# Optimization experiments

Hardware: AMD Instinct MI355X
Metric: run time of the kernel (lower is better)

## Reference

```python
import jax, jax.numpy as jnp
import numpy as np

DIM = 2048
NUM_HEADS = 16
HEAD_DIM = DIM // NUM_HEADS
FF_MULT = 2
ROPE_BASE = 10000.0
EPS = 1e-6


def _rmsnorm(x, g):
    return x * jax.lax.rsqrt(jnp.mean(x * x, axis=-1, keepdims=True) + EPS) * g


def _rope_tables(seq_len):
    half = HEAD_DIM // 2
    inv_freq = 1.0 / (ROPE_BASE ** (2.0 * jnp.arange(half, dtype=jnp.float32) / HEAD_DIM))
    angles = jnp.arange(seq_len, dtype=jnp.float32)[:, None] * inv_freq[None, :]  # (S, half)
    return jnp.cos(angles), jnp.sin(angles)


def _apply_rope(x, cos, sin):
    # x: (B, H, S, D); cos/sin: (S, D/2). Interleaved pairs (RoFormer form).
    x_even = x[..., 0::2]
    x_odd = x[..., 1::2]
    c = cos[None, None].astype(x.dtype)
    s = sin[None, None].astype(x.dtype)
    rot_even = x_even * c - x_odd * s
    rot_odd = x_odd * c + x_even * s
    return jnp.stack([rot_even, rot_odd], axis=-1).reshape(x.shape)


def setup_inputs() -> dict:
    key = jax.random.key(0)
    ks = jax.random.split(key, 7)
    B, S = 2, 2048
    scale = 1.0 / np.sqrt(DIM)
    return {
        "x": jax.random.normal(ks[0], (B, S, DIM), dtype=jnp.float32),
        "w_qkv": jax.random.normal(ks[1], (DIM, 3 * DIM), dtype=jnp.float32) * scale,
        "w_out": jax.random.normal(ks[2], (DIM, DIM), dtype=jnp.float32) * scale,
        "w_fc": jax.random.normal(ks[3], (DIM, DIM * FF_MULT), dtype=jnp.float32) * scale,
        "w_proj": jax.random.normal(ks[4], (DIM * FF_MULT, DIM), dtype=jnp.float32) / np.sqrt(DIM * FF_MULT),
        "g_in": jnp.ones((DIM,), dtype=jnp.float32),
        "g_ff": jnp.ones((DIM,), dtype=jnp.float32),
    }


def reference(x, w_qkv, w_out, w_fc, w_proj, g_in, g_ff):
    B, S, D = x.shape
    # --- attention branch ---
    h = _rmsnorm(x, g_in)
    qkv = h @ w_qkv  # (B, S, 3D)
    q, k, v = jnp.split(qkv, 3, axis=-1)
    def heads(t):
        return t.reshape(B, S, NUM_HEADS, HEAD_DIM).transpose(0, 2, 1, 3)
    q, k, v = heads(q), heads(k), heads(v)  # (B, H, S, Dh)
    cos, sin = _rope_tables(S)
    q = _apply_rope(q, cos, sin)
    k = _apply_rope(k, cos, sin)
    scores = jnp.einsum("bhqd,bhkd->bhqk", q, k) / jnp.asarray(np.sqrt(HEAD_DIM), x.dtype)
    causal = jnp.tril(jnp.ones((S, S), dtype=bool))
    scores = jnp.where(causal[None, None], scores, jnp.asarray(-jnp.inf, scores.dtype))
    attn = jax.nn.softmax(scores, axis=-1)
    out = jnp.einsum("bhqk,bhkd->bhqd", attn, v)  # (B, H, S, Dh)
    out = out.transpose(0, 2, 1, 3).reshape(B, S, D)
    x = x + out @ w_out
    # --- feed-forward branch ---
    h = _rmsnorm(x, g_ff)
    x = x + jax.nn.gelu(h @ w_fc) @ w_proj
    return x


if __name__ == "__main__":
    inp = setup_inputs()
    y = reference(**inp)
    print(y.shape, y.dtype)
```

## Files before the change

### kernel.cpp

```cpp
#include <hip/hip_runtime.h>
#include <math.h>

typedef __bf16 bf16x8 __attribute__((ext_vector_type(8)));
typedef float  f32x4  __attribute__((ext_vector_type(4)));

#define DEV __device__ __forceinline__

DEV void gload16(const void* g, void* l) {
  __builtin_amdgcn_global_load_lds(
      (const __attribute__((address_space(1))) void*)g,
      (__attribute__((address_space(3))) void*)l, 16, 0, 0);
}

__global__ __launch_bounds__(256) void transpose_cvt(
    const float* __restrict__ in, __bf16* __restrict__ outT, int R, int C) {
  __shared__ float t[32][33];
  const int c0 = blockIdx.x * 32, r0 = blockIdx.y * 32;
  const int tx = threadIdx.x, ty = threadIdx.y;
#pragma unroll
  for (int i = 0; i < 4; i++)
    t[ty + 8 * i][tx] = in[(size_t)(r0 + ty + 8 * i) * C + c0 + tx];
  __syncthreads();
#pragma unroll
  for (int i = 0; i < 4; i++)
    outT[(size_t)(c0 + ty + 8 * i) * R + r0 + tx] = (__bf16)t[tx][ty + 8 * i];
}

__global__ __launch_bounds__(256) void rmsnorm_kernel(
    const float* __restrict__ x, const float* __restrict__ g, __bf16* __restrict__ out) {
  const int r = blockIdx.x, t = threadIdx.x;
  const float4* xr = (const float4*)(x + (size_t)r * 2048);
  float4 a = xr[2 * t], b = xr[2 * t + 1];
  float ss = a.x * a.x + a.y * a.y + a.z * a.z + a.w * a.w +
             b.x * b.x + b.y * b.y + b.z * b.z + b.w * b.w;
#pragma unroll
  for (int mk = 1; mk < 64; mk <<= 1) ss += __shfl_xor(ss, mk);
  __shared__ float red[4];
  if ((t & 63) == 0) red[t >> 6] = ss;
  __syncthreads();
  const float sc = rsqrtf((red[0] + red[1] + red[2] + red[3]) * (1.0f / 2048.0f) + 1e-6f);
  const float4* gr = (const float4*)g;
  float4 ga = gr[2 * t], gb = gr[2 * t + 1];
  bf16x8 ov;
  ov[0] = (__bf16)(a.x * sc * ga.x); ov[1] = (__bf16)(a.y * sc * ga.y);
  ov[2] = (__bf16)(a.z * sc * ga.z); ov[3] = (__bf16)(a.w * sc * ga.w);
  ov[4] = (__bf16)(b.x * sc * gb.x); ov[5] = (__bf16)(b.y * sc * gb.y);
  ov[6] = (__bf16)(b.z * sc * gb.z); ov[7] = (__bf16)(b.w * sc * gb.w);
  *(bf16x8*)(out + (size_t)r * 2048 + t * 8) = ov;
}

template <int EPI>
__global__ __launch_bounds__(256) void gemm_bt(
    const __bf16* __restrict__ A, const __bf16* __restrict__ BT,
    void* __restrict__ Cout, const float* __restrict__ res, int M, int N, int K) {
  __shared__ char lds[32768];
  char* As = lds;
  char* Bs = lds + 16384;
  const int tid = threadIdx.x;
  const int lane = tid & 63;
  const int bn = blockIdx.x, bm = blockIdx.y;
  const int wm = tid >> 7, wn = (tid >> 6) & 1;

  f32x4 acc[4][4];
#pragma unroll
  for (int i = 0; i < 4; i++)
#pragma unroll
    for (int j = 0; j < 4; j++) acc[i][j] = (f32x4){0.f, 0.f, 0.f, 0.f};

  const size_t strideA = (size_t)K * 2;
  const char* ga[4];
  const char* gb[4];
#pragma unroll
  for (int t = 0; t < 4; t++) {
    int gg = t * 256 + tid;
    int row = gg >> 3, slot = gg & 7;
    ga[t] = (const char*)A + (size_t)(bm * 128 + row) * strideA + ((slot ^ (row & 7)) << 4);
    gb[t] = (const char*)BT + (size_t)(bn * 128 + row) * strideA + ((slot ^ (row & 7)) << 4);
  }

  for (int k0 = 0; k0 < K; k0 += 64) {
    __syncthreads();
#pragma unroll
    for (int t = 0; t < 4; t++) {
      int gg = t * 256 + tid;
      gload16(ga[t], As + gg * 16);
      gload16(gb[t], Bs + gg * 16);
      ga[t] += 128;
      gb[t] += 128;
    }
    __syncthreads();
#pragma unroll
    for (int kk = 0; kk < 2; kk++) {
      bf16x8 a[4], b[4];
      const int c16 = kk * 4 + (lane >> 4);
#pragma unroll
      for (int i = 0; i < 4; i++) {
        int ra = wm * 64 + i * 16 + (lane & 15);
        a[i] = *(const bf16x8*)(As + ra * 128 + ((c16 ^ (ra & 7)) << 4));
        int rb = wn * 64 + i * 16 + (lane & 15);
        b[i] = *(const bf16x8*)(Bs + rb * 128 + ((c16 ^ (rb & 7)) << 4));
      }
#pragma unroll
      for (int i = 0; i < 4; i++)
#pragma unroll
        for (int j = 0; j < 4; j++)
          acc[i][j] = __builtin_amdgcn_mfma_f32_16x16x32_bf16(a[i], b[j], acc[i][j], 0, 0, 0);
    }
  }

#pragma unroll
  for (int i = 0; i < 4; i++)
#pragma unroll
    for (int j = 0; j < 4; j++)
#pragma unroll
      for (int r = 0; r < 4; r++) {
        int row = bm * 128 + wm * 64 + i * 16 + ((lane >> 4) << 2) + r;
        int col = bn * 128 + wn * 64 + j * 16 + (lane & 15);
        size_t idx = (size_t)row * N + col;
        float v = acc[i][j][r];
        if (EPI == 0) {
          ((__bf16*)Cout)[idx] = (__bf16)v;
        } else if (EPI == 1) {
          ((float*)Cout)[idx] = v + res[idx];
        } else {
          float u = 0.7978845608028654f * (v + 0.044715f * v * v * v);
          ((__bf16*)Cout)[idx] = (__bf16)(0.5f * v * (1.0f + tanhf(u)));
        }
      }
}

__global__ __launch_bounds__(256) void rope_tables(float* __restrict__ tab) {
  const int idx = blockIdx.x * 256 + threadIdx.x;
  const int s = idx >> 6, j = idx & 63;
  const float inv = powf(10000.0f, -(float)j / 64.0f);
  const float a = (float)s * inv;
  tab[idx] = cosf(a);
  tab[131072 + idx] = sinf(a);
}

__global__ __launch_bounds__(256) void rope_apply(
    const __bf16* __restrict__ qkv, const float* __restrict__ tab,
    __bf16* __restrict__ qr, __bf16* __restrict__ kr) {
  const int idx = blockIdx.x * 256 + threadIdx.x;
  const int j = idx & 63;
  const int h = (idx >> 6) & 15;
  const int s = (idx >> 10) & 2047;
  const int b = idx >> 21;
  const float c = tab[(s << 6) + j], sn = tab[131072 + (s << 6) + j];
  const size_t qi = ((size_t)(b * 2048 + s)) * 6144 + h * 128 + 2 * j;
  const size_t qo = ((size_t)((b * 16 + h) * 2048 + s)) * 128 + 2 * j;
  {
    float e = (float)qkv[qi], o = (float)qkv[qi + 1];
    qr[qo] = (__bf16)(e * c - o * sn);
    qr[qo + 1] = (__bf16)(o * c + e * sn);
  }
  {
    float e = (float)qkv[qi + 2048], o = (float)qkv[qi + 2048 + 1];
    kr[qo] = (__bf16)(e * c - o * sn);
    kr[qo + 1] = (__bf16)(o * c + e * sn);
  }
}

__global__ __launch_bounds__(256) void v_transpose(
    const __bf16* __restrict__ qkv, __bf16* __restrict__ vt) {
  __shared__ __bf16 t[32][33];
  const int s0 = blockIdx.x * 32, d0 = blockIdx.y * 32, bh = blockIdx.z;
  const int b = bh >> 4, h = bh & 15;
  const int tx = threadIdx.x, ty = threadIdx.y;
#pragma unroll
  for (int i = 0; i < 4; i++)
    t[ty + 8 * i][tx] =
        qkv[((size_t)(b * 2048 + s0 + ty + 8 * i)) * 6144 + 4096 + h * 128 + d0 + tx];
  __syncthreads();
#pragma unroll
  for (int i = 0; i < 4; i++)
    vt[((size_t)bh * 128 + d0 + ty + 8 * i) * 2048 + s0 + tx] = t[tx][ty + 8 * i];
}

__global__ __launch_bounds__(512) void flash_attn(
    const __bf16* __restrict__ qg, const __bf16* __restrict__ kg,
    const __bf16* __restrict__ vtg, __bf16* __restrict__ og) {
  __shared__ char lds[81920];
  const int tid = threadIdx.x, lane = tid & 63, w = tid >> 6;
  const int h = blockIdx.y, b = blockIdx.z;
  const int bh = b * 16 + h;
  const __bf16* qb = qg + (size_t)bh * 2048 * 128;
  const char* kbb = (const char*)(kg + (size_t)bh * 2048 * 128);
  const char* vbb = (const char*)(vtg + (size_t)bh * 128 * 2048);
  char* Pw = lds + 65536 + w * 2048;

  const char* gK[2];
  const char* gV[2];
#pragma unroll
  for (int t = 0; t < 2; t++) {
    int gg = t * 512 + tid;
    int rk = gg >> 4, sk = gg & 15;
    gK[t] = kbb + rk * 256 + ((sk ^ (rk & 15)) << 4);
    int rv = gg >> 3, sv = gg & 7;
    gV[t] = vbb + rv * 4096 + ((sv ^ (rv & 7)) << 4);
  }

  const float SL2E = 0.08838834764831845f * 1.4426950408889634f;

  auto stageKV = [&](int kt, int buf) {
#pragma unroll
    for (int t = 0; t < 2; t++) {
      int gg = t * 512 + tid;
      gload16(gK[t] + (size_t)kt * 16384, lds + buf * 16384 + gg * 16);
      gload16(gV[t] + (size_t)kt * 128, lds + 32768 + buf * 16384 + gg * 16);
    }
  };

  auto run_qtile = [&](int qt) {
    const int qrow0 = qt * 128 + w * 16;
    bf16x8 qf[4];
#pragma unroll
    for (int c = 0; c < 4; c++) {
      bf16x8 raw = *(const bf16x8*)(qb + (size_t)(qrow0 + (lane & 15)) * 128 +
                                    c * 32 + ((lane >> 4) << 3));
#pragma unroll
      for (int e = 0; e < 8; e++) qf[c][e] = (__bf16)((float)raw[e] * SL2E);
    }
    float m[4], lsp[4];
    f32x4 o[8];
#pragma unroll
    for (int r = 0; r < 4; r++) { m[r] = -__builtin_inff(); lsp[r] = 0.f; }
#pragma unroll
    for (int n = 0; n < 8; n++) o[n] = (f32x4){0.f, 0.f, 0.f, 0.f};

    const int NKT = 2 * qt + 2;
    stageKV(0, 0);

    for (int kt = 0; kt < NKT; kt++) {
      const int cur = kt & 1;
      const char* Ks = lds + cur * 16384;
      const char* Vs = lds + 32768 + cur * 16384;
      if (kt < NKT - 1) {
        stageKV(kt + 1, cur ^ 1);
        asm volatile("s_waitcnt vmcnt(4)" ::: "memory");
      } else {
        asm volatile("s_waitcnt vmcnt(0)" ::: "memory");
      }
      __builtin_amdgcn_s_barrier();

      f32x4 s[4];
      __builtin_amdgcn_s_setprio(1);
#pragma unroll
      for (int n = 0; n < 4; n++) {
        s[n] = (f32x4){0.f, 0.f, 0.f, 0.f};
#pragma unroll
        for (int c = 0; c < 4; c++) {
          int krow = n * 16 + (lane & 15);
          int c16 = c * 4 + (lane >> 4);
          bf16x8 kf = *(const bf16x8*)(Ks + krow * 256 + ((c16 ^ (krow & 15)) << 4));
          s[n] = __builtin_amdgcn_mfma_f32_16x16x32_bf16(qf[c], kf, s[n], 0, 0, 0);
        }
      }
      __builtin_amdgcn_s_setprio(0);

      if (kt * 64 + 63 > qrow0) {
#pragma unroll
        for (int r = 0; r < 4; r++) {
          const int qrow = qrow0 + ((lane >> 4) << 2) + r;
#pragma unroll
          for (int n = 0; n < 4; n++) {
            int col = kt * 64 + n * 16 + (lane & 15);
            if (col > qrow) s[n][r] = -__builtin_inff();
          }
        }
      }

      float tmx[4];
#pragma unroll
      for (int r = 0; r < 4; r++)
        tmx[r] = fmaxf(fmaxf(s[0][r], s[1][r]), fmaxf(s[2][r], s[3][r]));
      bool hot = (tmx[0] > m[0] + 8.f) | (tmx[1] > m[1] + 8.f) |
                 (tmx[2] > m[2] + 8.f) | (tmx[3] > m[3] + 8.f);
      if (__any(hot)) {
        float fc[4];
#pragma unroll
        for (int r = 0; r < 4; r++) {
          float gmx = tmx[r];
#pragma unroll
          for (int mk = 1; mk < 16; mk <<= 1) gmx = fmaxf(gmx, __shfl_xor(gmx, mk));
          float nm = fmaxf(m[r], gmx);
          fc[r] = __builtin_amdgcn_exp2f(m[r] - nm);
          m[r] = nm;
          lsp[r] *= fc[r];
        }
#pragma unroll
        for (int n = 0; n < 8; n++) {
          o[n][0] *= fc[0]; o[n][1] *= fc[1]; o[n][2] *= fc[2]; o[n][3] *= fc[3];
        }
      }

      float p[4][4];
#pragma unroll
      for (int r = 0; r < 4; r++) {
        float sum = 0.f;
#pragma unroll
        for (int n = 0; n < 4; n++) {
          float pv = __builtin_amdgcn_exp2f(s[n][r] - m[r]);
          p[n][r] = pv;
          sum += pv;
        }
        lsp[r] += sum;
      }

#pragma unroll
      for (int n = 0; n < 4; n++)
#pragma unroll
        for (int r = 0; r < 4; r++) {
          int prow = ((lane >> 4) << 2) + r;
          int col = n * 16 + (lane & 15);
          int ch = col >> 3;
          *(__bf16*)(Pw + prow * 128 + ((ch ^ (prow & 7)) << 4) + ((col & 7) << 1)) =
              (__bf16)p[n][r];
        }

      __builtin_amdgcn_s_setprio(1);
#pragma unroll
      for (int kk = 0; kk < 2; kk++) {
        int prow = lane & 15;
        int pc = kk * 4 + (lane >> 4);
        bf16x8 pf = *(const bf16x8*)(Pw + prow * 128 + ((pc ^ (prow & 7)) << 4));
#pragma unroll
        for (int n = 0; n < 8; n++) {
          int vr = n * 16 + (lane & 15);
          bf16x8 vf = *(const bf16x8*)(Vs + vr * 128 + ((pc ^ (vr & 7)) << 4));
          o[n] = __builtin_amdgcn_mfma_f32_16x16x32_bf16(pf, vf, o[n], 0, 0, 0);
        }
      }
      __builtin_amdgcn_s_setprio(0);
      __builtin_amdgcn_s_barrier();
    }

    float inv[4];
#pragma unroll
    for (int r = 0; r < 4; r++) {
      float ls = lsp[r];
#pragma unroll
      for (int mk = 1; mk < 16; mk <<= 1) ls += __shfl_xor(ls, mk);
      inv[r] = 1.0f / ls;
    }
#pragma unroll
    for (int n = 0; n < 8; n++)
#pragma unroll
      for (int r = 0; r < 4; r++) {
        int qrow = qrow0 + ((lane >> 4) << 2) + r;
        og[(size_t)(b * 2048 + qrow) * 2048 + h * 128 + n * 16 + (lane & 15)] =
            (__bf16)(o[n][r] * inv[r]);
      }
  };

  run_qtile(15 - (int)blockIdx.x);
  run_qtile((int)blockIdx.x);
}

extern "C" void kernel_launch(void* const* d_in, const int* in_sizes, int n_in,
                              void* d_out, int out_size, void* d_ws, size_t ws_size,
                              hipStream_t stream) {
  const float* x = (const float*)d_in[0];
  const float* w_qkv = (const float*)d_in[1];
  const float* w_out = (const float*)d_in[2];
  const float* w_fc = (const float*)d_in[3];
  const float* w_proj = (const float*)d_in[4];
  const float* g_in = (const float*)d_in[5];
  const float* g_ff = (const float*)d_in[6];
  float* out = (float*)d_out;
  char* ws = (char*)d_ws;

  constexpr size_t O_WQKV = 0;
  constexpr size_t O_WOUT = 25165824;
  constexpr size_t O_WFC = 33554432;
  constexpr size_t O_WPROJ = 50331648;
  constexpr size_t O_H = 67108864;
  constexpr size_t O_QKV = 83886080;
  constexpr size_t O_Q = 134217728;
  constexpr size_t O_K = 150994944;
  constexpr size_t O_VT = 167772160;
  constexpr size_t O_TAB = 184549376;
  constexpr size_t O_ATTN = 185597952;
  constexpr size_t O_X1 = 202375168;

  __bf16* wqkvT = (__bf16*)(ws + O_WQKV);
  __bf16* woutT = (__bf16*)(ws + O_WOUT);
  __bf16* wfcT = (__bf16*)(ws + O_WFC);
  __bf16* wprojT = (__bf16*)(ws + O_WPROJ);
  __bf16* h = (__bf16*)(ws + O_H);
  __bf16* qkv = (__bf16*)(ws + O_QKV);
  __bf16* fcact = (__bf16*)(ws + O_QKV);
  __bf16* qr = (__bf16*)(ws + O_Q);
  __bf16* kr = (__bf16*)(ws + O_K);
  __bf16* vt = (__bf16*)(ws + O_VT);
  float* tab = (float*)(ws + O_TAB);
  __bf16* attn = (__bf16*)(ws + O_ATTN);
  float* x1 = (float*)(ws + O_X1);

  const dim3 tb(32, 8);
  transpose_cvt<<<dim3(6144 / 32, 2048 / 32), tb, 0, stream>>>(w_qkv, wqkvT, 2048, 6144);
  transpose_cvt<<<dim3(2048 / 32, 2048 / 32), tb, 0, stream>>>(w_out, woutT, 2048, 2048);
  transpose_cvt<<<dim3(4096 / 32, 2048 / 32), tb, 0, stream>>>(w_fc, wfcT, 2048, 4096);
  transpose_cvt<<<dim3(2048 / 32, 4096 / 32), tb, 0, stream>>>(w_proj, wprojT, 4096, 2048);

  rmsnorm_kernel<<<4096, 256, 0, stream>>>(x, g_in, h);
  gemm_bt<0><<<dim3(48, 32), 256, 0, stream>>>(h, wqkvT, (void*)qkv, nullptr, 4096, 6144, 2048);
  rope_tables<<<512, 256, 0, stream>>>(tab);
  rope_apply<<<16384, 256, 0, stream>>>(qkv, tab, qr, kr);
  v_transpose<<<dim3(64, 4, 32), tb, 0, stream>>>(qkv, vt);
  flash_attn<<<dim3(8, 16, 2), 512, 0, stream>>>(qr, kr, vt, attn);
  gemm_bt<1><<<dim3(16, 32), 256, 0, stream>>>(attn, woutT, (void*)x1, x, 4096, 2048, 2048);
  rmsnorm_kernel<<<4096, 256, 0, stream>>>(x1, g_ff, h);
  gemm_bt<2><<<dim3(32, 32), 256, 0, stream>>>(h, wfcT, (void*)fcact, nullptr, 4096, 4096, 2048);
  gemm_bt<1><<<dim3(16, 32), 256, 0, stream>>>(fcact, wprojT, (void*)out, x1, 4096, 2048, 4096);
}
```

Before: 520.9 us.

## Add 256x256-tile ping-pong GEMM kernel for QKV and FC projections

Adds a new GEMM kernel that uses 256x256 output tiles, 512 threads in 8 waves, and 128KB of double-buffered LDS. Waves alternate between loading fragments and issuing MFMA, with s_setprio and barriers enforcing the ping-pong schedule, and global_load_lds prefetches two k-tiles ahead. The QKV and FC GEMMs switch to this kernel. The aim is more data reuse per tile and better overlap of memory with MFMA work. In exchange, the grid has fewer blocks (384 and 256), which may leave CUs idle, and register pressure is high.

```diff
diff --git a/kernel.cpp b/kernel.cpp
--- a/kernel.cpp
+++ b/kernel.cpp
@@ -116,6 +116,135 @@
       for (int r = 0; r < 4; r++) {
         int row = bm * 128 + wm * 64 + i * 16 + ((lane >> 4) << 2) + r;
         int col = bn * 128 + wn * 64 + j * 16 + (lane & 15);
+        size_t idx = (size_t)row * N + col;
+        float v = acc[i][j][r];
+        if (EPI == 0) {
+          ((__bf16*)Cout)[idx] = (__bf16)v;
+        } else if (EPI == 1) {
+          ((float*)Cout)[idx] = v + res[idx];
+        } else {
+          float u = 0.7978845608028654f * (v + 0.044715f * v * v * v);
+          ((__bf16*)Cout)[idx] = (__bf16)(0.5f * v * (1.0f + tanhf(u)));
+        }
+      }
+}
+
+#define MMQ(IB, JB, AR, BR)                                                   \
+  __builtin_amdgcn_s_setprio(1);                                              \
+  _Pragma("unroll") for (int i = 0; i < 4; i++)                               \
+      _Pragma("unroll") for (int j = 0; j < 2; j++)                           \
+          _Pragma("unroll") for (int kk = 0; kk < 2; kk++)                    \
+              acc[(IB)*4 + i][(JB)*2 + j] =                                   \
+      __builtin_amdgcn_mfma_f32_16x16x32_bf16(                                \
+          AR[i][kk], BR[j][kk], acc[(IB)*4 + i][(JB)*2 + j], 0, 0, 0);        \
+  __builtin_amdgcn_s_setprio(0);
+
+template <int EPI>
+__global__ __launch_bounds__(512, 2) void gemm256(
+    const __bf16* __restrict__ A, const __bf16* __restrict__ BT,
+    void* __restrict__ Cout, const float* __restrict__ res, int M, int N, int K) {
+  __shared__ char lds[131072];
+  const int tid = threadIdx.x, lane = tid & 63, w = tid >> 6;
+  const int wm = w >> 2, wn = w & 3;
+  const int bn = blockIdx.x, bm = blockIdx.y;
+
+  f32x4 acc[8][4];
+#pragma unroll
+  for (int i = 0; i < 8; i++)
+#pragma unroll
+    for (int j = 0; j < 4; j++) acc[i][j] = (f32x4){0.f, 0.f, 0.f, 0.f};
+
+  const size_t strideA = (size_t)K * 2;
+  const int r0 = tid >> 3, s0 = tid & 7;
+  const int r1 = r0 + 64;
+  const char* Ab0 = (const char*)A + (size_t)(bm * 256) * strideA;
+  const char* Bb0 = (const char*)BT + (size_t)(bn * 256) * strideA;
+
+  auto stage = [&](int isB, int h, int kt, int buf) {
+    const char* g = (isB ? Bb0 : Ab0) + (size_t)(h * 128) * strideA + (size_t)kt * 128;
+    char* d = lds + isB * 65536 + buf * 32768 + h * 16384;
+    gload16(g + (size_t)r0 * strideA + ((s0 ^ (r0 & 7)) << 4), d + tid * 16);
+    gload16(g + (size_t)r1 * strideA + ((s0 ^ (r1 & 7)) << 4), d + (tid + 512) * 16);
+  };
+  auto ldA = [&](bf16x8 (&a)[4][2], int buf, int bank) {
+    const char* base = lds + buf * 32768 + wm * 16384;
+#pragma unroll
+    for (int i = 0; i < 4; i++)
+#pragma unroll
+      for (int kk = 0; kk < 2; kk++) {
+        int rl = bank * 64 + i * 16 + (lane & 15);
+        int c16 = kk * 4 + (lane >> 4);
+        a[i][kk] = *(const bf16x8*)(base + rl * 128 + ((c16 ^ (rl & 7)) << 4));
+      }
+  };
+  auto ldB = [&](bf16x8 (&b)[2][2], int buf, int jb) {
+    const char* base = lds + 65536 + buf * 32768 + (wn >> 1) * 16384;
+#pragma unroll
+    for (int j = 0; j < 2; j++)
+#pragma unroll
+      for (int kk = 0; kk < 2; kk++) {
+        int rl = (wn & 1) * 64 + jb * 32 + j * 16 + (lane & 15);
+        int c16 = kk * 4 + (lane >> 4);
+        b[j][kk] = *(const bf16x8*)(base + rl * 128 + ((c16 ^ (rl & 7)) << 4));
+      }
+  };
+
+  const int NT = K >> 6;
+  stage(1, 0, 0, 0); stage(1, 1, 0, 0); stage(0, 0, 0, 0); stage(0, 1, 0, 0);
+  stage(1, 0, 1, 1); stage(1, 1, 1, 1); stage(0, 0, 1, 1); stage(0, 1, 1, 1);
+  asm volatile("s_waitcnt vmcnt(6)" ::: "memory");
+  __builtin_amdgcn_s_barrier();
+
+  bf16x8 a[4][2], b0[2][2], b1[2][2];
+  for (int it = 0; it < (NT >> 1); ++it) {
+    const int e = 2 * it;
+    const int ep = (e + 2 < NT) ? e + 2 : NT - 1;
+    const int op = (e + 3 < NT) ? e + 3 : NT - 1;
+    ldA(a, 0, 0); ldB(b0, 0, 0);
+    __builtin_amdgcn_s_barrier();
+    MMQ(0, 0, a, b0);
+    __builtin_amdgcn_s_barrier();
+    ldB(b1, 0, 1);
+    __builtin_amdgcn_s_barrier();
+    MMQ(0, 1, a, b1);
+    __builtin_amdgcn_s_barrier();
+    ldA(a, 0, 1); stage(1, 0, ep, 0);
+    __builtin_amdgcn_s_barrier();
+    MMQ(1, 1, a, b1);
+    __builtin_amdgcn_s_barrier();
+    stage(1, 1, ep, 0);
+    asm volatile("s_waitcnt vmcnt(4)" ::: "memory");
+    __builtin_amdgcn_s_barrier();
+    MMQ(1, 0, a, b0);
+    __builtin_amdgcn_s_barrier();
+    ldA(a, 1, 0); ldB(b0, 1, 0); stage(0, 0, ep, 0);
+    __builtin_amdgcn_s_barrier();
+    MMQ(0, 0, a, b0);
+    __builtin_amdgcn_s_barrier();
+    ldB(b1, 1, 1); stage(0, 1, ep, 0);
+    __builtin_amdgcn_s_barrier();
+    MMQ(0, 1, a, b1);
+    __builtin_amdgcn_s_barrier();
+    ldA(a, 1, 1); stage(1, 0, op, 1);
+    __builtin_amdgcn_s_barrier();
+    MMQ(1, 1, a, b1);
+    __builtin_amdgcn_s_barrier();
+    stage(1, 1, op, 1); stage(0, 0, op, 1); stage(0, 1, op, 1);
+    asm volatile("s_waitcnt vmcnt(6)" ::: "memory");
+    __builtin_amdgcn_s_barrier();
+    MMQ(1, 0, a, b0);
+    __builtin_amdgcn_s_barrier();
+  }
+  asm volatile("s_waitcnt vmcnt(0)" ::: "memory");
+
+#pragma unroll
+  for (int i = 0; i < 8; i++)
+#pragma unroll
+    for (int j = 0; j < 4; j++)
+#pragma unroll
+      for (int r = 0; r < 4; r++) {
+        int row = bm * 256 + wm * 128 + i * 16 + ((lane >> 4) << 2) + r;
+        int col = bn * 256 + wn * 64 + j * 16 + (lane & 15);
         size_t idx = (size_t)row * N + col;
         float v = acc[i][j][r];
         if (EPI == 0) {
@@ -404,13 +533,13 @@
   transpose_cvt<<<dim3(2048 / 32, 4096 / 32), tb, 0, stream>>>(w_proj, wprojT, 4096, 2048);
 
   rmsnorm_kernel<<<4096, 256, 0, stream>>>(x, g_in, h);
-  gemm_bt<0><<<dim3(48, 32), 256, 0, stream>>>(h, wqkvT, (void*)qkv, nullptr, 4096, 6144, 2048);
+  gemm256<0><<<dim3(24, 16), 512, 0, stream>>>(h, wqkvT, (void*)qkv, nullptr, 4096, 6144, 2048);
   rope_tables<<<512, 256, 0, stream>>>(tab);
   rope_apply<<<16384, 256, 0, stream>>>(qkv, tab, qr, kr);
   v_transpose<<<dim3(64, 4, 32), tb, 0, stream>>>(qkv, vt);
   flash_attn<<<dim3(8, 16, 2), 512, 0, stream>>>(qr, kr, vt, attn);
   gemm_bt<1><<<dim3(16, 32), 256, 0, stream>>>(attn, woutT, (void*)x1, x, 4096, 2048, 2048);
   rmsnorm_kernel<<<4096, 256, 0, stream>>>(x1, g_ff, h);
-  gemm_bt<2><<<dim3(32, 32), 256, 0, stream>>>(h, wfcT, (void*)fcact, nullptr, 4096, 4096, 2048);
+  gemm256<2><<<dim3(16, 16), 512, 0, stream>>>(h, wfcT, (void*)fcact, nullptr, 4096, 4096, 2048);
   gemm_bt<1><<<dim3(16, 32), 256, 0, stream>>>(fcact, wprojT, (void*)out, x1, 4096, 2048, 4096);
 }
```

After: 518.1 us. No clear change (-0.5%).
